# Kernel tuning notes

Hardware: AMD Instinct MI355X
Metric: run time of the kernel (lower is better)

## Reference

```python
import jax, jax.numpy as jnp
import numpy as np

B, S, HID = 2, 2048, 2048
NH, NKV = 16, 4
HD = HID // NH            # 128
N_REP = NH // NKV          # 4
THETA = 10000.0
NEG = -1e9


def _rope_tables(position_ids):
    # inv_freq: [HD/2]
    inv_freq = 1.0 / (THETA ** (jnp.arange(0, HD, 2, dtype=jnp.float32) / HD))
    freqs = position_ids.astype(jnp.float32)[..., None] * inv_freq  # [B,S,HD/2]
    emb = jnp.concatenate([freqs, freqs], axis=-1)                  # [B,S,HD]
    return jnp.cos(emb), jnp.sin(emb)


def _rotate_half(x):
    return jnp.concatenate([-x[..., HD // 2:], x[..., :HD // 2]], axis=-1)


def setup_inputs() -> dict:
    key = jax.random.key(0)
    k1, k2, k3 = jax.random.split(key, 3)
    hidden_states = jax.random.normal(k1, (B, S, HID), dtype=jnp.float32)
    w_qkv = jax.random.normal(k2, (HID + 2 * NKV * HD, HID), dtype=jnp.float32) * 0.02
    w_out = jax.random.normal(k3, (HID, HID), dtype=jnp.float32) * 0.02
    causal = jnp.tril(jnp.ones((S, S), dtype=bool))
    attention_mask = jnp.where(causal, 0.0, NEG).astype(jnp.float32)
    attention_mask = jnp.broadcast_to(attention_mask[None, None], (B, 1, S, S))
    position_ids = jnp.broadcast_to(jnp.arange(S, dtype=jnp.int64), (B, S))
    return {"hidden_states": hidden_states, "w_qkv": w_qkv, "w_out": w_out,
            "attention_mask": attention_mask, "position_ids": position_ids}


def reference(hidden_states, w_qkv, w_out, attention_mask, position_ids):
    bsz, q_len, _ = hidden_states.shape
    qkv = hidden_states @ w_qkv.T                                   # [B,S,HID+2*NKV*HD]
    q, k, v = jnp.split(qkv, [HID, HID + NKV * HD], axis=-1)
    q = q.reshape(bsz, q_len, NH, HD).transpose(0, 2, 1, 3)         # [B,NH,S,HD]
    k = k.reshape(bsz, q_len, NKV, HD).transpose(0, 2, 1, 3)        # [B,NKV,S,HD]
    v = v.reshape(bsz, q_len, NKV, HD).transpose(0, 2, 1, 3)

    cos, sin = _rope_tables(position_ids)                           # [B,S,HD]
    cos, sin = cos[:, None], sin[:, None]                           # unsqueeze head dim
    q = q * cos + _rotate_half(q) * sin
    k = k * cos + _rotate_half(k) * sin

    # GQA: repeat KV heads to match query heads (repeat_kv)
    k = jnp.repeat(k, N_REP, axis=1)                                # [B,NH,S,HD]
    v = jnp.repeat(v, N_REP, axis=1)

    scale = 1.0 / jnp.sqrt(jnp.float32(HD))
    scores = jnp.einsum('bhqd,bhkd->bhqk', q, k) * scale
    scores = scores + attention_mask                                # [B,NH,S,S]
    attn = jax.nn.softmax(scores.astype(jnp.float32), axis=-1).astype(q.dtype)
    out = jnp.einsum('bhqk,bhkd->bhqd', attn, v)                    # [B,NH,S,HD]
    out = out.transpose(0, 2, 1, 3).reshape(bsz, q_len, HID)
    return out @ w_out.T
```

## Files before the change

kernel.cpp:

```cpp
#include <hip/hip_runtime.h>
#include <hip/hip_bf16.h>
#include <math.h>

#define S_LEN   2048
#define HIDDEN  2048
#define NHEADS  16
#define NKVH    4
#define HDIM    128

typedef short  short8  __attribute__((ext_vector_type(8)));
typedef float  floatx4 __attribute__((ext_vector_type(4)));
typedef __hip_bfloat16 bf16;

__device__ inline void async_copy16(const void* g, void* l) {
  __builtin_amdgcn_global_load_lds((__attribute__((address_space(1))) void*)(g),
                                   (__attribute__((address_space(3))) void*)(l),
                                   16, 0, 0);
}

__device__ inline unsigned short cvt1(float x) {
  bf16 t = __float2bfloat16(x);
  return *reinterpret_cast<unsigned short*>(&t);
}
__device__ inline float us2f(unsigned short u) {
  unsigned int v = ((unsigned int)u) << 16;
  return *reinterpret_cast<float*>(&v);
}

#define N8_H  1048576
#define N8_WQ  786432
#define N8_WO  524288
__global__ __launch_bounds__(256) void cvt_all(const float* __restrict__ h,
                                               const float* __restrict__ wq,
                                               const float* __restrict__ wo,
                                               unsigned short* __restrict__ dst) {
  const int i = blockIdx.x * 256 + threadIdx.x;
  if (i >= N8_H + N8_WQ + N8_WO) return;
  const float* src; int j;
  if (i < N8_H)              { src = h;  j = i; }
  else if (i < N8_H + N8_WQ) { src = wq; j = i - N8_H; }
  else                       { src = wo; j = i - N8_H - N8_WQ; }
  const float4 a = reinterpret_cast<const float4*>(src)[j * 2];
  const float4 b = reinterpret_cast<const float4*>(src)[j * 2 + 1];
  unsigned short o[8] = {cvt1(a.x), cvt1(a.y), cvt1(a.z), cvt1(a.w),
                         cvt1(b.x), cvt1(b.y), cvt1(b.z), cvt1(b.w)};
  *reinterpret_cast<short8*>(dst + (size_t)i * 8) = *reinterpret_cast<short8*>(o);
}

template<int MODE>
__global__ __launch_bounds__(512, 2) void gemm8(const bf16* __restrict__ A,
                                                const bf16* __restrict__ B,
                                                bf16* __restrict__ qbuf,
                                                bf16* __restrict__ kbuf,
                                                bf16* __restrict__ vtbuf,
                                                float* __restrict__ Cout)
{
  constexpr int K      = 2048;
  constexpr int BM     = (MODE == 0) ? 256 : 128;
  constexpr int BN     = 256;
  constexpr int MF     = BM / 32;
  constexpr int AI     = BM / 128;
  constexpr int ABYTES = BM * 64;
  constexpr int SLOT   = (BM + BN) * 64;
  constexpr int NSTEP  = K / 32;

  __shared__ __align__(16) unsigned short smem[SLOT * 4 / 2];
  char* smb = (char*)smem;

  const int bn = blockIdx.x, bm = blockIdx.y;
  const int t = threadIdx.x, w = t >> 6, lane = t & 63;
  const int m16 = lane & 15, quad = lane >> 4;
  const int wmr = (w >> 2) * (BM / 2);
  const int wn  = w & 3;

  int bcol[4];
#pragma unroll
  for (int ni = 0; ni < 4; ++ni)
    bcol[ni] = (MODE == 0)
             ? ((wn >> 1) * 128 + (wn & 1) * 32 + (ni & 1) * 16 + (ni >> 1) * 64)
             : (wn * 64 + ni * 16);

  int afo[MF], bfo[4];
#pragma unroll
  for (int mf = 0; mf < MF; ++mf) {
    const int r = wmr + mf * 16 + m16;
    afo[mf] = r * 64 + ((quad ^ ((r >> 1) & 3)) << 4);
  }
#pragma unroll
  for (int ni = 0; ni < 4; ++ni) {
    const int r = bcol[ni] + m16;
    bfo[ni] = ABYTES + r * 64 + ((quad ^ ((r >> 1) & 3)) << 4);
  }

  const bf16* srcA[AI]; int dstA[AI];
#pragma unroll
  for (int j = 0; j < AI; ++j) {
    const int ci  = w * AI + j;
    const int row = ci * 16 + (lane >> 2);
    const int sl  = (lane & 3) ^ ((row >> 1) & 3);
    srcA[j] = A + (size_t)(bm * BM + row) * K + sl * 8;
    dstA[j] = ci * 1024;
  }
  const bf16* srcB[2]; int dstB[2];
#pragma unroll
  for (int j = 0; j < 2; ++j) {
    const int ci  = w * 2 + j;
    const int row = ci * 16 + (lane >> 2);
    const int sl  = (lane & 3) ^ ((row >> 1) & 3);
    srcB[j] = B + (size_t)(bn * BN + row) * K + sl * 8;
    dstB[j] = ABYTES + ci * 1024;
  }

  auto stage = [&](int step, int slotbyte) {
#pragma unroll
    for (int j = 0; j < AI; ++j)
      async_copy16(srcA[j] + step * 32, smb + slotbyte + dstA[j]);
#pragma unroll
    for (int j = 0; j < 2; ++j)
      async_copy16(srcB[j] + step * 32, smb + slotbyte + dstB[j]);
  };

  const floatx4 zf = {0.f, 0.f, 0.f, 0.f};
  floatx4 acc[MF][4];
#pragma unroll
  for (int mf = 0; mf < MF; ++mf)
#pragma unroll
    for (int ni = 0; ni < 4; ++ni) acc[mf][ni] = zf;

  stage(0, 0); stage(1, SLOT); stage(2, 2 * SLOT);

#pragma unroll 4
  for (int s = 0; s < NSTEP; ++s) {
    __builtin_amdgcn_sched_barrier(0);
    if constexpr (MODE == 0) asm volatile("s_waitcnt vmcnt(8)" ::: "memory");
    else                     asm volatile("s_waitcnt vmcnt(6)" ::: "memory");
    __builtin_amdgcn_s_barrier();
    __builtin_amdgcn_sched_barrier(0);
    const int sb = (s & 3) * SLOT;
    short8 af[MF], bfr[4];
#pragma unroll
    for (int mf = 0; mf < MF; ++mf)
      af[mf] = *reinterpret_cast<const short8*>(smb + sb + afo[mf]);
#pragma unroll
    for (int ni = 0; ni < 4; ++ni)
      bfr[ni] = *reinterpret_cast<const short8*>(smb + sb + bfo[ni]);
    stage((s + 3) & (NSTEP - 1), ((s + 3) & 3) * SLOT);
    __builtin_amdgcn_s_setprio(1);
#pragma unroll
    for (int mf = 0; mf < MF; ++mf)
#pragma unroll
      for (int ni = 0; ni < 4; ++ni)
        acc[mf][ni] = __builtin_amdgcn_mfma_f32_16x16x32_bf16(af[mf], bfr[ni], acc[mf][ni], 0, 0, 0);
    __builtin_amdgcn_s_setprio(0);
  }
  __builtin_amdgcn_s_waitcnt(0);

  if constexpr (MODE == 1) {
#pragma unroll
    for (int mf = 0; mf < MF; ++mf)
#pragma unroll
      for (int ni = 0; ni < 4; ++ni) {
        const int row0 = bm * BM + wmr + mf * 16 + quad * 4;
        const int col  = bn * BN + bcol[ni] + m16;
#pragma unroll
        for (int r = 0; r < 4; ++r)
          Cout[(size_t)(row0 + r) * HIDDEN + col] = acc[mf][ni][r];
      }
  } else {
    const int colbase = bn * BN;
    if (colbase < HIDDEN + NKVH * HDIM) {
      const bool isQ = (colbase < HIDDEN);
      const float post = isQ ? 0.08838834764831845f : 1.0f;
      float invf[2];
#pragma unroll
      for (int p = 0; p < 2; ++p)
        invf[p] = exp2f((float)((wn & 1) * 32 + p * 16 + m16) * -0.2076205059f);
#pragma unroll
      for (int mf = 0; mf < MF; ++mf) {
        const int row0 = bm * BM + wmr + mf * 16 + quad * 4;
#pragma unroll
        for (int r = 0; r < 4; ++r) {
          const int m = row0 + r;
          const int b = m >> 11, s = m & 2047;
          float sn[2], cs[2];
          __sincosf((float)s * invf[0], &sn[0], &cs[0]);
          __sincosf((float)s * invf[1], &sn[1], &cs[1]);
#pragma unroll
          for (int ni = 0; ni < 4; ++ni) {
            const int p = ni & 1;
            const float v  = acc[mf][ni][r];
            const float v2 = acc[mf][ni ^ 2][r];
            const float rot = ((ni < 2) ? (v * cs[p] - v2 * sn[p])
                                        : (v * cs[p] + v2 * sn[p])) * post;
            const int col = colbase + bcol[ni] + m16;
            if (isQ) {
              const int hh = col >> 7, d = col & 127;
              qbuf[(((size_t)(b * NHEADS + hh)) * S_LEN + s) * HDIM + d] = __float2bfloat16(rot);
            } else {
              const int nn = col - HIDDEN; const int hh = nn >> 7, d = nn & 127;
              kbuf[(((size_t)(b * NKVH + hh)) * S_LEN + s) * HDIM + d] = __float2bfloat16(rot);
            }
          }
        }
      }
    } else {
#pragma unroll
      for (int mf = 0; mf < MF; ++mf)
#pragma unroll
        for (int ni = 0; ni < 4; ++ni) {
          const int col = colbase + bcol[ni] + m16;
          const int nn = col - HIDDEN - NKVH * HDIM;
          const int hh = nn >> 7, d = nn & 127;
          const int row0 = bm * BM + wmr + mf * 16 + quad * 4;
#pragma unroll
          for (int r = 0; r < 4; ++r) {
            const int m = row0 + r;
            const int b = m >> 11, s = m & 2047;
            vtbuf[(((size_t)(b * NKVH + hh)) * HDIM + d) * S_LEN + s] =
                __float2bfloat16(acc[mf][ni][r]);
          }
        }
    }
  }
}

__global__ __launch_bounds__(256) void attn_partial(const bf16* __restrict__ qbuf,
                                                    const bf16* __restrict__ kbuf,
                                                    const bf16* __restrict__ vtbuf,
                                                    unsigned short* __restrict__ pnum,
                                                    float* __restrict__ plsum,
                                                    bf16* __restrict__ abuf)
{
  __shared__ unsigned short Ks[2][4096];
  __shared__ unsigned short Vs[2][4096];
  __shared__ unsigned short Ps[4][1280];
  const int sidx = 110 - blockIdx.x;
  int i2, c, nch;
  if (sidx < 27)      { i2 = sidx;                     c = 0;              nch = 1; }
  else if (sidx < 81) { i2 = 27 + ((sidx - 27) >> 1);  c = (sidx - 27) & 1; nch = 2; }
  else                { i2 = 54 + (sidx - 81) / 3;     c = (sidx - 81) % 3; nch = 3; }
  const int len = i2 + 1;
  const int k0 = (c * len) / nch, k1 = ((c + 1) * len) / nch;
  const int kvh = blockIdx.y, b = blockIdx.z;
  const int t = threadIdx.x, w = t >> 6, lane = t & 63;
  const int m16 = lane & 15, quad = lane >> 4;
  const int h = kvh * 4 + w;

  const bf16* Qp = qbuf + (((size_t)(b * NHEADS + h)) * S_LEN + i2 * 32 + m16) * HDIM;
  short8 qf[2][4];
#pragma unroll
  for (int T = 0; T < 2; ++T)
#pragma unroll
    for (int cc = 0; cc < 4; ++cc)
      qf[T][cc] = *reinterpret_cast<const short8*>(Qp + (size_t)T * 16 * HDIM + cc * 32 + quad * 8);

  const bf16* Kp  = kbuf  + ((size_t)(b * NKVH + kvh)) * S_LEN * HDIM;
  const bf16* Vtp = vtbuf + ((size_t)(b * NKVH + kvh)) * HDIM * S_LEN;

  const int kk = lane >> 4, cK = lane & 15;
  const int rKa = w * 8 + kk, rKb = rKa + 4;
  const int offKa = rKa * 128 + ((cK ^ (rKa & 7)) * 8);
  const int offKb = rKb * 128 + ((cK ^ (rKb & 7)) * 8);
  const int dd = lane >> 2, cV = lane & 3;
  const int dVa = w * 32 + dd, dVb = dVa + 16;
  const int offVa = dVa * 2048 + ((cV ^ ((dVa >> 1) & 3)) * 8);
  const int offVb = dVb * 2048 + ((cV ^ ((dVb >> 1) & 3)) * 8);

  const floatx4 zf = {0.f, 0.f, 0.f, 0.f};
  floatx4 oacc[2][8];
#pragma unroll
  for (int T = 0; T < 2; ++T)
#pragma unroll
    for (int d = 0; d < 8; ++d) oacc[T][d] = zf;
  floatx4 lacc[2] = {zf, zf};
  unsigned short ones_s[8] = {0x3F80,0x3F80,0x3F80,0x3F80,0x3F80,0x3F80,0x3F80,0x3F80};
  const short8 ones = *reinterpret_cast<short8*>(ones_s);

  unsigned short* Pw = &Ps[w][0];

  {
    const int ks = k0 * 32;
    async_copy16(Kp + (size_t)ks * 128 + offKa, &Ks[0][w * 1024]);
    async_copy16(Kp + (size_t)ks * 128 + offKb, &Ks[0][w * 1024 + 512]);
    async_copy16(Vtp + ks + offVa, &Vs[0][w * 1024]);
    async_copy16(Vtp + ks + offVb, &Vs[0][w * 1024 + 512]);
  }
  __syncthreads();

  for (int ki = k0; ki < k1; ++ki) {
    const int buf = (ki - k0) & 1;
    if (ki + 1 < k1) {
      const int ks = (ki + 1) * 32;
      async_copy16(Kp + (size_t)ks * 128 + offKa, &Ks[buf ^ 1][w * 1024]);
      async_copy16(Kp + (size_t)ks * 128 + offKb, &Ks[buf ^ 1][w * 1024 + 512]);
      async_copy16(Vtp + ks + offVa, &Vs[buf ^ 1][w * 1024]);
      async_copy16(Vtp + ks + offVb, &Vs[buf ^ 1][w * 1024 + 512]);
    }
    const int ks = ki * 32;
    floatx4 s00 = zf, s01 = zf, s10 = zf, s11 = zf;
#pragma unroll
    for (int cc = 0; cc < 4; ++cc) {
      const int sw = ((cc * 4 + quad) ^ (m16 & 7)) * 8;
      short8 kf0 = *reinterpret_cast<const short8*>(&Ks[buf][m16 * 128 + sw]);
      short8 kf1 = *reinterpret_cast<const short8*>(&Ks[buf][(16 + m16) * 128 + sw]);
      s00 = __builtin_amdgcn_mfma_f32_16x16x32_bf16(qf[0][cc], kf0, s00, 0, 0, 0);
      s01 = __builtin_amdgcn_mfma_f32_16x16x32_bf16(qf[0][cc], kf1, s01, 0, 0, 0);
      s10 = __builtin_amdgcn_mfma_f32_16x16x32_bf16(qf[1][cc], kf0, s10, 0, 0, 0);
      s11 = __builtin_amdgcn_mfma_f32_16x16x32_bf16(qf[1][cc], kf1, s11, 0, 0, 0);
    }
#pragma unroll
    for (int T = 0; T < 2; ++T) {
      const floatx4& sa = T ? s10 : s00;
      const floatx4& sb = T ? s11 : s01;
#pragma unroll
      for (int r = 0; r < 4; ++r) {
        const int row = i2 * 32 + T * 16 + quad * 4 + r;
        const float p0 = (ks + m16      > row) ? 0.f : __expf(sa[r]);
        const float p1 = (ks + 16 + m16 > row) ? 0.f : __expf(sb[r]);
        Pw[(T * 16 + quad * 4 + r) * 40 + m16]      = cvt1(p0);
        Pw[(T * 16 + quad * 4 + r) * 40 + 16 + m16] = cvt1(p1);
      }
    }
    const short8 pa0 = *reinterpret_cast<const short8*>(&Pw[m16 * 40 + quad * 8]);
    const short8 pa1 = *reinterpret_cast<const short8*>(&Pw[(16 + m16) * 40 + quad * 8]);
    lacc[0] = __builtin_amdgcn_mfma_f32_16x16x32_bf16(pa0, ones, lacc[0], 0, 0, 0);
    lacc[1] = __builtin_amdgcn_mfma_f32_16x16x32_bf16(pa1, ones, lacc[1], 0, 0, 0);
#pragma unroll
    for (int dt = 0; dt < 8; ++dt) {
      short8 vfr = *reinterpret_cast<const short8*>(
          &Vs[buf][(dt * 16 + m16) * 32 + ((quad ^ ((m16 >> 1) & 3)) * 8)]);
      oacc[0][dt] = __builtin_amdgcn_mfma_f32_16x16x32_bf16(pa0, vfr, oacc[0][dt], 0, 0, 0);
      oacc[1][dt] = __builtin_amdgcn_mfma_f32_16x16x32_bf16(pa1, vfr, oacc[1][dt], 0, 0, 0);
    }
    __syncthreads();
  }

  if (nch == 1) {
#pragma unroll
    for (int T = 0; T < 2; ++T) {
      float invl[4];
#pragma unroll
      for (int r = 0; r < 4; ++r) invl[r] = 1.0f / lacc[T][r];
      bf16* op = abuf + (((size_t)b * S_LEN + i2 * 32 + T * 16 + quad * 4) * NHEADS + h) * HDIM + m16;
#pragma unroll
      for (int dt = 0; dt < 8; ++dt)
#pragma unroll
        for (int r = 0; r < 4; ++r)
          op[(size_t)r * NHEADS * HDIM + dt * 16] = __float2bfloat16(oacc[T][dt][r] * invl[r]);
    }
  } else {
    const int b0 = (i2 < 54) ? (27 + 2 * (i2 - 27)) : (81 + 3 * (i2 - 54));
    const int slot = (b * NHEADS + h) * 111 + b0 + c;
    unsigned short* np = pnum + (size_t)slot * 4096;
#pragma unroll
    for (int T = 0; T < 2; ++T)
#pragma unroll
      for (int dt = 0; dt < 8; ++dt)
#pragma unroll
        for (int r = 0; r < 4; ++r)
          np[(T * 16 + quad * 4 + r) * 128 + dt * 16 + m16] = cvt1(oacc[T][dt][r]);
    if (m16 == 0) {
#pragma unroll
      for (int T = 0; T < 2; ++T)
#pragma unroll
        for (int r = 0; r < 4; ++r)
          plsum[slot * 32 + T * 16 + quad * 4 + r] = lacc[T][r];
    }
  }
}

__global__ __launch_bounds__(256) void attn_combine(const unsigned short* __restrict__ pnum,
                                                    const float* __restrict__ plsum,
                                                    bf16* __restrict__ abuf)
{
  const int i = 54 + blockIdx.x;
  const int h = blockIdx.y, b = blockIdx.z;
  const int i2 = i >> 1, lr0 = (i & 1) * 16;
  const int t = threadIdx.x, row16 = t >> 4, c0 = (t & 15) * 8;
  const int lr = lr0 + row16;
  const int nch = (i2 < 54) ? 2 : 3;
  const int b0  = (i2 < 54) ? (27 + 2 * (i2 - 27)) : (81 + 3 * (i2 - 54));
  const int hb = (b * NHEADS + h) * 111 + b0;
  float acc[8] = {0.f,0.f,0.f,0.f,0.f,0.f,0.f,0.f};
  float lsum = 0.f;
  for (int c = 0; c < nch; ++c) {
    const unsigned short* np = pnum + (size_t)(hb + c) * 4096 + lr * 128 + c0;
    const short8 v = *reinterpret_cast<const short8*>(np);
#pragma unroll
    for (int j = 0; j < 8; ++j) acc[j] += us2f(((unsigned short*)&v)[j]);
    lsum += plsum[(hb + c) * 32 + lr];
  }
  const float invl = 1.0f / lsum;
  unsigned short o[8];
#pragma unroll
  for (int j = 0; j < 8; ++j) o[j] = cvt1(acc[j] * invl);
  *reinterpret_cast<short8*>(abuf + (((size_t)b * S_LEN + i * 16 + row16) * NHEADS + h) * HDIM + c0)
      = *reinterpret_cast<short8*>(o);
}

extern "C" void kernel_launch(void* const* d_in, const int* in_sizes, int n_in,
                              void* d_out, int out_size, void* d_ws, size_t ws_size,
                              hipStream_t stream) {
  const float* hidden_f = (const float*)d_in[0];
  const float* wqkv_f   = (const float*)d_in[1];
  const float* wout_f   = (const float*)d_in[2];
  float* out = (float*)d_out;

  char* ws = (char*)d_ws;
  bf16* hbf    = (bf16*)(ws);
  bf16* wqkvbf = (bf16*)(ws + 16777216);
  bf16* woutbf = (bf16*)(ws + 29360128);
  bf16* qbuf   = (bf16*)(ws + 37748736);
  bf16* kbuf   = (bf16*)(ws + 54525952);
  bf16* vtbuf  = (bf16*)(ws + 58720256);
  bf16* abuf   = (bf16*)(ws + 62914560);
  unsigned short* pnum = (unsigned short*)(ws);
  float* plsum = (float*)(ws + 79691776);

  cvt_all<<<9216, 256, 0, stream>>>(hidden_f, wqkv_f, wout_f, (unsigned short*)ws);

  gemm8<0><<<dim3(12, 16), 512, 0, stream>>>(hbf, wqkvbf, qbuf, kbuf, vtbuf, nullptr);
  attn_partial<<<dim3(111, 4, 2), 256, 0, stream>>>(qbuf, kbuf, vtbuf, pnum, plsum, abuf);
  attn_combine<<<dim3(74, 16, 2), 256, 0, stream>>>(pnum, plsum, abuf);
  gemm8<1><<<dim3(8, 32), 512, 0, stream>>>(abuf, woutbf, nullptr, nullptr, nullptr, out);
}
```

Before: 302.7 us.

## Double query rows per attention block to reuse K/V tiles across 64 queries

Each attention_partial block now processes 64 query rows per head instead of 32, with a repartitioned split-K chunk schedule (63 blocks per kv-head instead of 111) and matching slot layout for partial numerators and row sums in the combine kernel. Each K/V tile loaded into shared memory feeds twice as many MFMAs, which cuts global/LDS traffic per unit of work. The trade-off is more accumulator registers (launch bounds set to one block), fewer blocks in the grid (504 total) and coarser causal-triangle load balancing.

```diff
diff --git a/kernel.cpp b/kernel.cpp
--- a/kernel.cpp
+++ b/kernel.cpp
@@ -224,32 +224,32 @@
   }
 }
 
-__global__ __launch_bounds__(256) void attn_partial(const bf16* __restrict__ qbuf,
-                                                    const bf16* __restrict__ kbuf,
-                                                    const bf16* __restrict__ vtbuf,
-                                                    unsigned short* __restrict__ pnum,
-                                                    float* __restrict__ plsum,
-                                                    bf16* __restrict__ abuf)
+__global__ __launch_bounds__(256, 1) void attn_partial(const bf16* __restrict__ qbuf,
+                                                       const bf16* __restrict__ kbuf,
+                                                       const bf16* __restrict__ vtbuf,
+                                                       unsigned short* __restrict__ pnum,
+                                                       float* __restrict__ plsum,
+                                                       bf16* __restrict__ abuf)
 {
   __shared__ unsigned short Ks[2][4096];
   __shared__ unsigned short Vs[2][4096];
-  __shared__ unsigned short Ps[4][1280];
-  const int sidx = 110 - blockIdx.x;
-  int i2, c, nch;
-  if (sidx < 27)      { i2 = sidx;                     c = 0;              nch = 1; }
-  else if (sidx < 81) { i2 = 27 + ((sidx - 27) >> 1);  c = (sidx - 27) & 1; nch = 2; }
-  else                { i2 = 54 + (sidx - 81) / 3;     c = (sidx - 81) % 3; nch = 3; }
-  const int len = i2 + 1;
+  __shared__ unsigned short Ps[4][2560];
+  const int sidx = 62 - blockIdx.x;
+  int i4, c, nch;
+  if (sidx < 11)      { i4 = sidx;                 c = 0;              nch = 1; }
+  else if (sidx < 33) { i4 = 11 + ((sidx - 11) >> 1); c = (sidx - 11) & 1; nch = 2; }
+  else                { i4 = 22 + (sidx - 33) / 3;    c = (sidx - 33) % 3; nch = 3; }
+  const int len = 2 * (i4 + 1);
   const int k0 = (c * len) / nch, k1 = ((c + 1) * len) / nch;
   const int kvh = blockIdx.y, b = blockIdx.z;
   const int t = threadIdx.x, w = t >> 6, lane = t & 63;
   const int m16 = lane & 15, quad = lane >> 4;
   const int h = kvh * 4 + w;
 
-  const bf16* Qp = qbuf + (((size_t)(b * NHEADS + h)) * S_LEN + i2 * 32 + m16) * HDIM;
-  short8 qf[2][4];
-#pragma unroll
-  for (int T = 0; T < 2; ++T)
+  const bf16* Qp = qbuf + (((size_t)(b * NHEADS + h)) * S_LEN + i4 * 64 + m16) * HDIM;
+  short8 qf[4][4];
+#pragma unroll
+  for (int T = 0; T < 4; ++T)
 #pragma unroll
     for (int cc = 0; cc < 4; ++cc)
       qf[T][cc] = *reinterpret_cast<const short8*>(Qp + (size_t)T * 16 * HDIM + cc * 32 + quad * 8);
@@ -267,12 +267,12 @@
   const int offVb = dVb * 2048 + ((cV ^ ((dVb >> 1) & 3)) * 8);
 
   const floatx4 zf = {0.f, 0.f, 0.f, 0.f};
-  floatx4 oacc[2][8];
-#pragma unroll
-  for (int T = 0; T < 2; ++T)
+  floatx4 oacc[4][8];
+#pragma unroll
+  for (int T = 0; T < 4; ++T)
 #pragma unroll
     for (int d = 0; d < 8; ++d) oacc[T][d] = zf;
-  floatx4 lacc[2] = {zf, zf};
+  floatx4 lacc[4] = {zf, zf, zf, zf};
   unsigned short ones_s[8] = {0x3F80,0x3F80,0x3F80,0x3F80,0x3F80,0x3F80,0x3F80,0x3F80};
   const short8 ones = *reinterpret_cast<short8*>(ones_s);
 
@@ -297,51 +297,54 @@
       async_copy16(Vtp + ks + offVb, &Vs[buf ^ 1][w * 1024 + 512]);
     }
     const int ks = ki * 32;
-    floatx4 s00 = zf, s01 = zf, s10 = zf, s11 = zf;
+    floatx4 sA[4] = {zf, zf, zf, zf}, sB[4] = {zf, zf, zf, zf};
 #pragma unroll
     for (int cc = 0; cc < 4; ++cc) {
       const int sw = ((cc * 4 + quad) ^ (m16 & 7)) * 8;
       short8 kf0 = *reinterpret_cast<const short8*>(&Ks[buf][m16 * 128 + sw]);
       short8 kf1 = *reinterpret_cast<const short8*>(&Ks[buf][(16 + m16) * 128 + sw]);
-      s00 = __builtin_amdgcn_mfma_f32_16x16x32_bf16(qf[0][cc], kf0, s00, 0, 0, 0);
-      s01 = __builtin_amdgcn_mfma_f32_16x16x32_bf16(qf[0][cc], kf1, s01, 0, 0, 0);
-      s10 = __builtin_amdgcn_mfma_f32_16x16x32_bf16(qf[1][cc], kf0, s10, 0, 0, 0);
-      s11 = __builtin_amdgcn_mfma_f32_16x16x32_bf16(qf[1][cc], kf1, s11, 0, 0, 0);
-    }
-#pragma unroll
-    for (int T = 0; T < 2; ++T) {
-      const floatx4& sa = T ? s10 : s00;
-      const floatx4& sb = T ? s11 : s01;
+#pragma unroll
+      for (int T = 0; T < 4; ++T) {
+        sA[T] = __builtin_amdgcn_mfma_f32_16x16x32_bf16(qf[T][cc], kf0, sA[T], 0, 0, 0);
+        sB[T] = __builtin_amdgcn_mfma_f32_16x16x32_bf16(qf[T][cc], kf1, sB[T], 0, 0, 0);
+      }
+    }
+#pragma unroll
+    for (int T = 0; T < 4; ++T) {
 #pragma unroll
       for (int r = 0; r < 4; ++r) {
-        const int row = i2 * 32 + T * 16 + quad * 4 + r;
-        const float p0 = (ks + m16      > row) ? 0.f : __expf(sa[r]);
-        const float p1 = (ks + 16 + m16 > row) ? 0.f : __expf(sb[r]);
+        const int row = i4 * 64 + T * 16 + quad * 4 + r;
+        const float p0 = (ks + m16      > row) ? 0.f : __expf(sA[T][r]);
+        const float p1 = (ks + 16 + m16 > row) ? 0.f : __expf(sB[T][r]);
         Pw[(T * 16 + quad * 4 + r) * 40 + m16]      = cvt1(p0);
         Pw[(T * 16 + quad * 4 + r) * 40 + 16 + m16] = cvt1(p1);
       }
     }
-    const short8 pa0 = *reinterpret_cast<const short8*>(&Pw[m16 * 40 + quad * 8]);
-    const short8 pa1 = *reinterpret_cast<const short8*>(&Pw[(16 + m16) * 40 + quad * 8]);
-    lacc[0] = __builtin_amdgcn_mfma_f32_16x16x32_bf16(pa0, ones, lacc[0], 0, 0, 0);
-    lacc[1] = __builtin_amdgcn_mfma_f32_16x16x32_bf16(pa1, ones, lacc[1], 0, 0, 0);
+    short8 pa[4];
+#pragma unroll
+    for (int T = 0; T < 4; ++T)
+      pa[T] = *reinterpret_cast<const short8*>(&Pw[(T * 16 + m16) * 40 + quad * 8]);
+#pragma unroll
+    for (int T = 0; T < 4; ++T)
+      lacc[T] = __builtin_amdgcn_mfma_f32_16x16x32_bf16(pa[T], ones, lacc[T], 0, 0, 0);
 #pragma unroll
     for (int dt = 0; dt < 8; ++dt) {
       short8 vfr = *reinterpret_cast<const short8*>(
           &Vs[buf][(dt * 16 + m16) * 32 + ((quad ^ ((m16 >> 1) & 3)) * 8)]);
-      oacc[0][dt] = __builtin_amdgcn_mfma_f32_16x16x32_bf16(pa0, vfr, oacc[0][dt], 0, 0, 0);
-      oacc[1][dt] = __builtin_amdgcn_mfma_f32_16x16x32_bf16(pa1, vfr, oacc[1][dt], 0, 0, 0);
+#pragma unroll
+      for (int T = 0; T < 4; ++T)
+        oacc[T][dt] = __builtin_amdgcn_mfma_f32_16x16x32_bf16(pa[T], vfr, oacc[T][dt], 0, 0, 0);
     }
     __syncthreads();
   }
 
   if (nch == 1) {
 #pragma unroll
-    for (int T = 0; T < 2; ++T) {
+    for (int T = 0; T < 4; ++T) {
       float invl[4];
 #pragma unroll
       for (int r = 0; r < 4; ++r) invl[r] = 1.0f / lacc[T][r];
-      bf16* op = abuf + (((size_t)b * S_LEN + i2 * 32 + T * 16 + quad * 4) * NHEADS + h) * HDIM + m16;
+      bf16* op = abuf + (((size_t)b * S_LEN + i4 * 64 + T * 16 + quad * 4) * NHEADS + h) * HDIM + m16;
 #pragma unroll
       for (int dt = 0; dt < 8; ++dt)
 #pragma unroll
@@ -349,11 +352,11 @@
           op[(size_t)r * NHEADS * HDIM + dt * 16] = __float2bfloat16(oacc[T][dt][r] * invl[r]);
     }
   } else {
-    const int b0 = (i2 < 54) ? (27 + 2 * (i2 - 27)) : (81 + 3 * (i2 - 54));
-    const int slot = (b * NHEADS + h) * 111 + b0 + c;
-    unsigned short* np = pnum + (size_t)slot * 4096;
-#pragma unroll
-    for (int T = 0; T < 2; ++T)
+    const int base = (i4 <= 21) ? (i4 - 11) * 2 : 22 + (i4 - 22) * 3;
+    const int slot = (b * NHEADS + h) * 52 + base + c;
+    unsigned short* np = pnum + (size_t)slot * 8192;
+#pragma unroll
+    for (int T = 0; T < 4; ++T)
 #pragma unroll
       for (int dt = 0; dt < 8; ++dt)
 #pragma unroll
@@ -361,10 +364,10 @@
           np[(T * 16 + quad * 4 + r) * 128 + dt * 16 + m16] = cvt1(oacc[T][dt][r]);
     if (m16 == 0) {
 #pragma unroll
-      for (int T = 0; T < 2; ++T)
+      for (int T = 0; T < 4; ++T)
 #pragma unroll
         for (int r = 0; r < 4; ++r)
-          plsum[slot * 32 + T * 16 + quad * 4 + r] = lacc[T][r];
+          plsum[(size_t)slot * 64 + T * 16 + quad * 4 + r] = lacc[T][r];
     }
   }
 }
@@ -373,28 +376,29 @@
                                                     const float* __restrict__ plsum,
                                                     bf16* __restrict__ abuf)
 {
-  const int i = 54 + blockIdx.x;
+  const int bx = blockIdx.x;
+  const int i4 = 11 + (bx >> 2);
+  const int quarter = bx & 3;
   const int h = blockIdx.y, b = blockIdx.z;
-  const int i2 = i >> 1, lr0 = (i & 1) * 16;
+  const int nch  = (i4 <= 21) ? 2 : 3;
+  const int base = (i4 <= 21) ? (i4 - 11) * 2 : 22 + (i4 - 22) * 3;
+  const int hb = (b * NHEADS + h) * 52 + base;
   const int t = threadIdx.x, row16 = t >> 4, c0 = (t & 15) * 8;
-  const int lr = lr0 + row16;
-  const int nch = (i2 < 54) ? 2 : 3;
-  const int b0  = (i2 < 54) ? (27 + 2 * (i2 - 27)) : (81 + 3 * (i2 - 54));
-  const int hb = (b * NHEADS + h) * 111 + b0;
+  const int lr = quarter * 16 + row16;
   float acc[8] = {0.f,0.f,0.f,0.f,0.f,0.f,0.f,0.f};
   float lsum = 0.f;
   for (int c = 0; c < nch; ++c) {
-    const unsigned short* np = pnum + (size_t)(hb + c) * 4096 + lr * 128 + c0;
+    const unsigned short* np = pnum + (size_t)(hb + c) * 8192 + lr * 128 + c0;
     const short8 v = *reinterpret_cast<const short8*>(np);
 #pragma unroll
     for (int j = 0; j < 8; ++j) acc[j] += us2f(((unsigned short*)&v)[j]);
-    lsum += plsum[(hb + c) * 32 + lr];
+    lsum += plsum[(size_t)(hb + c) * 64 + lr];
   }
   const float invl = 1.0f / lsum;
   unsigned short o[8];
 #pragma unroll
   for (int j = 0; j < 8; ++j) o[j] = cvt1(acc[j] * invl);
-  *reinterpret_cast<short8*>(abuf + (((size_t)b * S_LEN + i * 16 + row16) * NHEADS + h) * HDIM + c0)
+  *reinterpret_cast<short8*>(abuf + (((size_t)b * S_LEN + i4 * 64 + lr) * NHEADS + h) * HDIM + c0)
       = *reinterpret_cast<short8*>(o);
 }
 
@@ -420,7 +424,7 @@
   cvt_all<<<9216, 256, 0, stream>>>(hidden_f, wqkv_f, wout_f, (unsigned short*)ws);
 
   gemm8<0><<<dim3(12, 16), 512, 0, stream>>>(hbf, wqkvbf, qbuf, kbuf, vtbuf, nullptr);
-  attn_partial<<<dim3(111, 4, 2), 256, 0, stream>>>(qbuf, kbuf, vtbuf, pnum, plsum, abuf);
-  attn_combine<<<dim3(74, 16, 2), 256, 0, stream>>>(pnum, plsum, abuf);
+  attn_partial<<<dim3(63, 4, 2), 256, 0, stream>>>(qbuf, kbuf, vtbuf, pnum, plsum, abuf);
+  attn_combine<<<dim3(84, 16, 2), 256, 0, stream>>>(pnum, plsum, abuf);
   gemm8<1><<<dim3(8, 32), 512, 0, stream>>>(abuf, woutbf, nullptr, nullptr, nullptr, out);
 }
```

After: 326.5 us. 1.08x slower.

## Deepen attention K/V prefetch to four-stage ring with explicit vmcnt waits

Applied to the files above, without the earlier changes.

Replaces the double-buffered K/V LDS pipeline in the attention kernel with a 4-slot ring that keeps three tiles in flight, using explicit s_waitcnt vmcnt(8) plus a single barrier per iteration instead of two syncthreads. Redundant clamped loads keep the in-flight count constant near the tail. It also raises wave priority around the MFMA sections. The aim is to hide global-load latency better, at the cost of doubling K/V LDS usage, which may reduce occupancy.

```diff
diff --git a/kernel.cpp b/kernel.cpp
--- a/kernel.cpp
+++ b/kernel.cpp
@@ -231,8 +231,8 @@
                                                     float* __restrict__ plsum,
                                                     bf16* __restrict__ abuf)
 {
-  __shared__ unsigned short Ks[2][4096];
-  __shared__ unsigned short Vs[2][4096];
+  __shared__ unsigned short Ks[4][4096];
+  __shared__ unsigned short Vs[4][4096];
   __shared__ unsigned short Ps[4][1280];
   const int sidx = 110 - blockIdx.x;
   int i2, c, nch;
@@ -278,36 +278,50 @@
 
   unsigned short* Pw = &Ps[w][0];
 
-  {
-    const int ks = k0 * 32;
-    async_copy16(Kp + (size_t)ks * 128 + offKa, &Ks[0][w * 1024]);
-    async_copy16(Kp + (size_t)ks * 128 + offKb, &Ks[0][w * 1024 + 512]);
-    async_copy16(Vtp + ks + offVa, &Vs[0][w * 1024]);
-    async_copy16(Vtp + ks + offVb, &Vs[0][w * 1024 + 512]);
-  }
-  __syncthreads();
+  __builtin_amdgcn_sched_barrier(0);
+  asm volatile("s_waitcnt vmcnt(0)" ::: "memory");
+  __builtin_amdgcn_sched_barrier(0);
+
+#pragma unroll
+  for (int j = 0; j < 3; ++j) {
+    const int kp = (k0 + j < k1) ? k0 + j : k1 - 1;
+    const int sl = (k0 + j) & 3;
+    const int ks = kp * 32;
+    async_copy16(Kp + (size_t)ks * 128 + offKa, &Ks[sl][w * 1024]);
+    async_copy16(Kp + (size_t)ks * 128 + offKb, &Ks[sl][w * 1024 + 512]);
+    async_copy16(Vtp + ks + offVa, &Vs[sl][w * 1024]);
+    async_copy16(Vtp + ks + offVb, &Vs[sl][w * 1024 + 512]);
+  }
 
   for (int ki = k0; ki < k1; ++ki) {
-    const int buf = (ki - k0) & 1;
-    if (ki + 1 < k1) {
-      const int ks = (ki + 1) * 32;
-      async_copy16(Kp + (size_t)ks * 128 + offKa, &Ks[buf ^ 1][w * 1024]);
-      async_copy16(Kp + (size_t)ks * 128 + offKb, &Ks[buf ^ 1][w * 1024 + 512]);
-      async_copy16(Vtp + ks + offVa, &Vs[buf ^ 1][w * 1024]);
-      async_copy16(Vtp + ks + offVb, &Vs[buf ^ 1][w * 1024 + 512]);
+    __builtin_amdgcn_sched_barrier(0);
+    asm volatile("s_waitcnt vmcnt(8)" ::: "memory");
+    __builtin_amdgcn_s_barrier();
+    __builtin_amdgcn_sched_barrier(0);
+    const int slot = ki & 3;
+    {
+      const int kf = (ki + 3 < k1) ? ki + 3 : k1 - 1;
+      const int sl = (ki + 3) & 3;
+      const int ks2 = kf * 32;
+      async_copy16(Kp + (size_t)ks2 * 128 + offKa, &Ks[sl][w * 1024]);
+      async_copy16(Kp + (size_t)ks2 * 128 + offKb, &Ks[sl][w * 1024 + 512]);
+      async_copy16(Vtp + ks2 + offVa, &Vs[sl][w * 1024]);
+      async_copy16(Vtp + ks2 + offVb, &Vs[sl][w * 1024 + 512]);
     }
     const int ks = ki * 32;
     floatx4 s00 = zf, s01 = zf, s10 = zf, s11 = zf;
+    __builtin_amdgcn_s_setprio(1);
 #pragma unroll
     for (int cc = 0; cc < 4; ++cc) {
       const int sw = ((cc * 4 + quad) ^ (m16 & 7)) * 8;
-      short8 kf0 = *reinterpret_cast<const short8*>(&Ks[buf][m16 * 128 + sw]);
-      short8 kf1 = *reinterpret_cast<const short8*>(&Ks[buf][(16 + m16) * 128 + sw]);
+      short8 kf0 = *reinterpret_cast<const short8*>(&Ks[slot][m16 * 128 + sw]);
+      short8 kf1 = *reinterpret_cast<const short8*>(&Ks[slot][(16 + m16) * 128 + sw]);
       s00 = __builtin_amdgcn_mfma_f32_16x16x32_bf16(qf[0][cc], kf0, s00, 0, 0, 0);
       s01 = __builtin_amdgcn_mfma_f32_16x16x32_bf16(qf[0][cc], kf1, s01, 0, 0, 0);
       s10 = __builtin_amdgcn_mfma_f32_16x16x32_bf16(qf[1][cc], kf0, s10, 0, 0, 0);
       s11 = __builtin_amdgcn_mfma_f32_16x16x32_bf16(qf[1][cc], kf1, s11, 0, 0, 0);
     }
+    __builtin_amdgcn_s_setprio(0);
 #pragma unroll
     for (int T = 0; T < 2; ++T) {
       const floatx4& sa = T ? s10 : s00;
@@ -323,17 +337,19 @@
     }
     const short8 pa0 = *reinterpret_cast<const short8*>(&Pw[m16 * 40 + quad * 8]);
     const short8 pa1 = *reinterpret_cast<const short8*>(&Pw[(16 + m16) * 40 + quad * 8]);
+    __builtin_amdgcn_s_setprio(1);
     lacc[0] = __builtin_amdgcn_mfma_f32_16x16x32_bf16(pa0, ones, lacc[0], 0, 0, 0);
     lacc[1] = __builtin_amdgcn_mfma_f32_16x16x32_bf16(pa1, ones, lacc[1], 0, 0, 0);
 #pragma unroll
     for (int dt = 0; dt < 8; ++dt) {
       short8 vfr = *reinterpret_cast<const short8*>(
-          &Vs[buf][(dt * 16 + m16) * 32 + ((quad ^ ((m16 >> 1) & 3)) * 8)]);
+          &Vs[slot][(dt * 16 + m16) * 32 + ((quad ^ ((m16 >> 1) & 3)) * 8)]);
       oacc[0][dt] = __builtin_amdgcn_mfma_f32_16x16x32_bf16(pa0, vfr, oacc[0][dt], 0, 0, 0);
       oacc[1][dt] = __builtin_amdgcn_mfma_f32_16x16x32_bf16(pa1, vfr, oacc[1][dt], 0, 0, 0);
     }
-    __syncthreads();
-  }
+    __builtin_amdgcn_s_setprio(0);
+  }
+  __builtin_amdgcn_s_waitcnt(0);
 
   if (nch == 1) {
 #pragma unroll
```

Result: slower. 314.4 us (+3.9%).

## Software-pipeline attention loop: overlap next tile QK with current softmax/PV

Applied to the files above, without the earlier changes.

Restructures the attention K/V loop so the QK^T MFMAs for tile k+1 are issued before the exp/P-store/PV work of tile k, unrolled by two with alternating score registers. K/V LDS staging grows from two to four slots and prefetches one tile further ahead. The aim is to hide softmax and LDS round-trip latency behind matrix work. In exchange, LDS per block rises a lot, which can lower occupancy, and register pressure grows from the extra score accumulators.

```diff
diff --git a/kernel.cpp b/kernel.cpp
--- a/kernel.cpp
+++ b/kernel.cpp
@@ -231,8 +231,8 @@
                                                     float* __restrict__ plsum,
                                                     bf16* __restrict__ abuf)
 {
-  __shared__ unsigned short Ks[2][4096];
-  __shared__ unsigned short Vs[2][4096];
+  __shared__ unsigned short Ks[4][4096];
+  __shared__ unsigned short Vs[4][4096];
   __shared__ unsigned short Ps[4][1280];
   const int sidx = 110 - blockIdx.x;
   int i2, c, nch;
@@ -278,36 +278,34 @@
 
   unsigned short* Pw = &Ps[w][0];
 
-  {
-    const int ks = k0 * 32;
-    async_copy16(Kp + (size_t)ks * 128 + offKa, &Ks[0][w * 1024]);
-    async_copy16(Kp + (size_t)ks * 128 + offKb, &Ks[0][w * 1024 + 512]);
-    async_copy16(Vtp + ks + offVa, &Vs[0][w * 1024]);
-    async_copy16(Vtp + ks + offVb, &Vs[0][w * 1024 + 512]);
-  }
-  __syncthreads();
-
-  for (int ki = k0; ki < k1; ++ki) {
-    const int buf = (ki - k0) & 1;
-    if (ki + 1 < k1) {
-      const int ks = (ki + 1) * 32;
-      async_copy16(Kp + (size_t)ks * 128 + offKa, &Ks[buf ^ 1][w * 1024]);
-      async_copy16(Kp + (size_t)ks * 128 + offKb, &Ks[buf ^ 1][w * 1024 + 512]);
-      async_copy16(Vtp + ks + offVa, &Vs[buf ^ 1][w * 1024]);
-      async_copy16(Vtp + ks + offVb, &Vs[buf ^ 1][w * 1024 + 512]);
-    }
-    const int ks = ki * 32;
-    floatx4 s00 = zf, s01 = zf, s10 = zf, s11 = zf;
+  auto stage_tile = [&](int kt) {
+    const int sl = kt & 3;
+    const int ks = kt * 32;
+    async_copy16(Kp + (size_t)ks * 128 + offKa, &Ks[sl][w * 1024]);
+    async_copy16(Kp + (size_t)ks * 128 + offKb, &Ks[sl][w * 1024 + 512]);
+    async_copy16(Vtp + ks + offVa, &Vs[sl][w * 1024]);
+    async_copy16(Vtp + ks + offVb, &Vs[sl][w * 1024 + 512]);
+  };
+
+  auto qk = [&](int kt, floatx4& s00, floatx4& s01, floatx4& s10, floatx4& s11) {
+    const int sl = kt & 3;
+    s00 = zf; s01 = zf; s10 = zf; s11 = zf;
 #pragma unroll
     for (int cc = 0; cc < 4; ++cc) {
       const int sw = ((cc * 4 + quad) ^ (m16 & 7)) * 8;
-      short8 kf0 = *reinterpret_cast<const short8*>(&Ks[buf][m16 * 128 + sw]);
-      short8 kf1 = *reinterpret_cast<const short8*>(&Ks[buf][(16 + m16) * 128 + sw]);
+      short8 kf0 = *reinterpret_cast<const short8*>(&Ks[sl][m16 * 128 + sw]);
+      short8 kf1 = *reinterpret_cast<const short8*>(&Ks[sl][(16 + m16) * 128 + sw]);
       s00 = __builtin_amdgcn_mfma_f32_16x16x32_bf16(qf[0][cc], kf0, s00, 0, 0, 0);
       s01 = __builtin_amdgcn_mfma_f32_16x16x32_bf16(qf[0][cc], kf1, s01, 0, 0, 0);
       s10 = __builtin_amdgcn_mfma_f32_16x16x32_bf16(qf[1][cc], kf0, s10, 0, 0, 0);
       s11 = __builtin_amdgcn_mfma_f32_16x16x32_bf16(qf[1][cc], kf1, s11, 0, 0, 0);
     }
+  };
+
+  auto finish = [&](int kt, const floatx4& s00, const floatx4& s01,
+                    const floatx4& s10, const floatx4& s11) {
+    const int sl = kt & 3;
+    const int ks = kt * 32;
 #pragma unroll
     for (int T = 0; T < 2; ++T) {
       const floatx4& sa = T ? s10 : s00;
@@ -328,11 +326,35 @@
 #pragma unroll
     for (int dt = 0; dt < 8; ++dt) {
       short8 vfr = *reinterpret_cast<const short8*>(
-          &Vs[buf][(dt * 16 + m16) * 32 + ((quad ^ ((m16 >> 1) & 3)) * 8)]);
+          &Vs[sl][(dt * 16 + m16) * 32 + ((quad ^ ((m16 >> 1) & 3)) * 8)]);
       oacc[0][dt] = __builtin_amdgcn_mfma_f32_16x16x32_bf16(pa0, vfr, oacc[0][dt], 0, 0, 0);
       oacc[1][dt] = __builtin_amdgcn_mfma_f32_16x16x32_bf16(pa1, vfr, oacc[1][dt], 0, 0, 0);
     }
+  };
+
+  stage_tile(k0);
+  if (k0 + 1 < k1) stage_tile(k0 + 1);
+  __syncthreads();
+  floatx4 a00, a01, a10, a11, b00, b01, b10, b11;
+  qk(k0, a00, a01, a10, a11);
+
+  int ki = k0 + 1;
+  for (; ki + 1 < k1; ki += 2) {
+    stage_tile(ki + 1);
+    qk(ki, b00, b01, b10, b11);
+    finish(ki - 1, a00, a01, a10, a11);
     __syncthreads();
+    if (ki + 2 < k1) stage_tile(ki + 2);
+    qk(ki + 1, a00, a01, a10, a11);
+    finish(ki, b00, b01, b10, b11);
+    __syncthreads();
+  }
+  if (ki < k1) {
+    qk(ki, b00, b01, b10, b11);
+    finish(ki - 1, a00, a01, a10, a11);
+    finish(ki, b00, b01, b10, b11);
+  } else {
+    finish(ki - 1, a00, a01, a10, a11);
   }
 
   if (nch == 1) {
```

New measurement: 305.2 us. About the same (+0.8%).
